# Optimization experiments

Hardware: AMD Instinct MI355X
Metric: run time of the kernel (lower is better)

Reference implementation:

```python
import jax, jax.numpy as jnp
import numpy as np

E4M3_MAX = 448.0
CHUNKS = 4  # module init: chunks=4, seg_mode='weight', equal chunksizes of out//chunks


def fp8_quant(v):
    # Simulate real e4m3 quantization: saturate then round-to-nearest e4m3, back to f32.
    return jnp.clip(v, -E4M3_MAX, E4M3_MAX).astype(jnp.float8_e4m3fn).astype(jnp.float32)


def setup_inputs() -> dict:
    key = jax.random.key(0)
    k1, k2, k3 = jax.random.split(key, 3)
    B, S, IN, OUT = 4, 4096, 4096, 4096
    x = jax.random.normal(k1, (B, S, IN), jnp.float32)
    w = jax.random.normal(k2, (OUT, IN), jnp.float32) * 0.02
    bias = jax.random.normal(k3, (OUT,), jnp.float32) * 0.01
    # Max-calibrated per-tensor scales (quantizer.scale from calibration)
    in_scale = jnp.max(jnp.abs(x)) / E4M3_MAX          # scalar
    wc = w.reshape(CHUNKS, OUT // CHUNKS, IN)
    w_scales = jnp.max(jnp.abs(wc), axis=(1, 2)) / E4M3_MAX  # [CHUNKS]
    return {"x": x, "w": w, "bias": bias, "in_scale": in_scale, "w_scales": w_scales}


def reference(x, w, bias, in_scale, w_scales):
    # seg_mode='weight': split weight along out_features into CHUNKS equal chunks,
    # run scaled e4m3 GEMM per chunk, concat outputs along out dim, add bias.
    OUT, IN = w.shape
    wc = w.reshape(CHUNKS, OUT // CHUNKS, IN)                 # [c, oc, i]
    xq = fp8_quant(x / in_scale)                              # [b, s, i]
    wq = fp8_quant(wc / w_scales[:, None, None])              # [c, oc, i]
    # out_i = (xq @ wq_i^T) * in_scale * w_scale_i  (dequant fused into GEMM epilogue)
    out = jnp.einsum('bsi,coi->bsco', xq, wq)
    out = out * (in_scale * w_scales)[None, None, :, None]
    out = out.reshape(x.shape[0], x.shape[1], OUT)            # concat chunk outputs
    return out + bias
```

## Files before the change

kernel.cpp:

```cpp
#include <hip/hip_runtime.h>
#include <stdint.h>

#define E4M3_MAX 448.0f

typedef float f32x4 __attribute__((ext_vector_type(4)));
typedef int   i32x4 __attribute__((ext_vector_type(4)));
typedef int   i32x8 __attribute__((ext_vector_type(8)));

__device__ __forceinline__ void gload_lds16(const void* g, void* l) {
    __builtin_amdgcn_global_load_lds(
        (__attribute__((address_space(1))) void*)(void*)g,
        (__attribute__((address_space(3))) void*)l,
        16, 0, 0);
}

__device__ __forceinline__ uint32_t quant4(float a, float b, float c, float d) {
    a = fminf(fmaxf(a, -E4M3_MAX), E4M3_MAX);
    b = fminf(fmaxf(b, -E4M3_MAX), E4M3_MAX);
    c = fminf(fmaxf(c, -E4M3_MAX), E4M3_MAX);
    d = fminf(fmaxf(d, -E4M3_MAX), E4M3_MAX);
    int q = 0;
    q = __builtin_amdgcn_cvt_pk_fp8_f32(a, b, q, false);
    q = __builtin_amdgcn_cvt_pk_fp8_f32(c, d, q, true);
    return (uint32_t)q;
}

__global__ void quant_x_kernel(const float* __restrict__ x,
                               const float* __restrict__ scale_p,
                               uint4* __restrict__ xq, int n16) {
    const float inv = 1.0f / scale_p[0];
    const int stride = gridDim.x * blockDim.x;
    for (int i = blockIdx.x * blockDim.x + threadIdx.x; i < n16; i += stride) {
        const float4* p = (const float4*)x + (size_t)i * 4;
        float4 v0 = p[0], v1 = p[1], v2 = p[2], v3 = p[3];
        uint4 q;
        q.x = quant4(v0.x * inv, v0.y * inv, v0.z * inv, v0.w * inv);
        q.y = quant4(v1.x * inv, v1.y * inv, v1.z * inv, v1.w * inv);
        q.z = quant4(v2.x * inv, v2.y * inv, v2.z * inv, v2.w * inv);
        q.w = quant4(v3.x * inv, v3.y * inv, v3.z * inv, v3.w * inv);
        xq[i] = q;
    }
}

__global__ void quant_w_kernel(const float* __restrict__ w,
                               const float* __restrict__ wsc,
                               uint4* __restrict__ wq, int n16, int chunk16) {
    const int stride = gridDim.x * blockDim.x;
    for (int i = blockIdx.x * blockDim.x + threadIdx.x; i < n16; i += stride) {
        const float inv = 1.0f / wsc[i / chunk16];
        const float4* p = (const float4*)w + (size_t)i * 4;
        float4 v0 = p[0], v1 = p[1], v2 = p[2], v3 = p[3];
        uint4 q;
        q.x = quant4(v0.x * inv, v0.y * inv, v0.z * inv, v0.w * inv);
        q.y = quant4(v1.x * inv, v1.y * inv, v1.z * inv, v1.w * inv);
        q.z = quant4(v2.x * inv, v2.y * inv, v2.z * inv, v2.w * inv);
        q.w = quant4(v3.x * inv, v3.y * inv, v3.z * inv, v3.w * inv);
        wq[i] = q;
    }
}

__device__ __forceinline__ i32x8 read_frag(const uint8_t* base, int o0, int o1) {
    i32x4 lo = *(const i32x4*)(base + o0);
    i32x4 hi = *(const i32x4*)(base + o1);
    return __builtin_shufflevector(lo, hi, 0, 1, 2, 3, 4, 5, 6, 7);
}

#define MFMA_MX(a, b, c) \
    __builtin_amdgcn_mfma_scale_f32_16x16x128_f8f6f4( \
        (a), (b), (c), 0, 0, 0, 0x7F7F7F7F, 0, 0x7F7F7F7F)

#define BM 256
#define BN 256
#define BKB 128

__global__ __launch_bounds__(512, 2) void gemm_fp8_kernel(
    const uint8_t* __restrict__ Aq, const uint8_t* __restrict__ Bq,
    const float* __restrict__ bias, const float* __restrict__ isp,
    const float* __restrict__ wsc, float* __restrict__ out,
    int M, int N, int K, int ocPerChunk) {
    __shared__ __align__(16) uint8_t lds[2][2][BM * BKB];

    const int tid  = threadIdx.x;
    const int lane = tid & 63;
    const int wid  = tid >> 6;
    const int wm   = wid >> 2;
    const int wn   = wid & 3;

    const int nwg = gridDim.x;
    const int cpx = nwg >> 3;
    const int swz = (blockIdx.x & 7) * cpx + (blockIdx.x >> 3);
    const int nbx = N / BN;
    const int bx  = swz % nbx;
    const int by  = swz / nbx;
    const int m0  = by * BM;
    const int n0  = bx * BN;

    const int lr   = lane & 15;
    const int sw   = (lr & 7) << 4;
    const int off0 = ((lane >> 4) * 32) ^ sw;
    const int off1 = off0 ^ 16;

    f32x4 acc[8][4] = {};

    const int nkt = K / BKB;

    auto stage = [&](int b, int kt) {
#pragma unroll
        for (int i = 0; i < 8; ++i) {
            const int idx = i * 512 + tid;
            const int row = idx >> 3;
            const int col = ((idx & 7) * 16) ^ ((row & 7) << 4);
            const uint8_t* src = (i < 4)
                ? Aq + (size_t)(m0 + row) * K + kt + col
                : Bq + (size_t)(n0 + (row - 256)) * K + kt + col;
            gload_lds16(src, &lds[b][0][0] + idx * 16);
        }
    };

    stage(0, 0);
    asm volatile("s_waitcnt vmcnt(0)" ::: "memory");
    __builtin_amdgcn_s_barrier();

    for (int t = 0; t < nkt; ++t) {
        const int cur = t & 1;
        const uint8_t* pa = &lds[cur][0][0] + (wm * 128 + lr) * BKB;
        const uint8_t* pb = &lds[cur][1][0] + (wn * 64  + lr) * BKB;

        i32x8 bv[4];
#pragma unroll
        for (int ni = 0; ni < 4; ni++)
            bv[ni] = read_frag(pb + ni * 16 * BKB, off0, off1);
        i32x8 a0 = read_frag(pa,            off0, off1);
        i32x8 a1 = read_frag(pa + 16 * BKB, off0, off1);
        if (t + 1 < nkt) stage(cur ^ 1, (t + 1) * BKB);

        __builtin_amdgcn_s_barrier();
        asm volatile("s_waitcnt lgkmcnt(0)" ::: "memory");
        __builtin_amdgcn_sched_barrier(0);
        __builtin_amdgcn_s_setprio(1);
#pragma unroll
        for (int ni = 0; ni < 4; ni++) {
            acc[0][ni] = MFMA_MX(a0, bv[ni], acc[0][ni]);
            acc[1][ni] = MFMA_MX(a1, bv[ni], acc[1][ni]);
        }
        __builtin_amdgcn_s_setprio(0);

#pragma unroll
        for (int p = 1; p < 4; ++p) {
            i32x8 c0 = read_frag(pa + (2 * p)     * 16 * BKB, off0, off1);
            i32x8 c1 = read_frag(pa + (2 * p + 1) * 16 * BKB, off0, off1);
            __builtin_amdgcn_s_barrier();
            asm volatile("s_waitcnt lgkmcnt(0)" ::: "memory");
            __builtin_amdgcn_sched_barrier(0);
            __builtin_amdgcn_s_setprio(1);
#pragma unroll
            for (int ni = 0; ni < 4; ni++) {
                acc[2 * p][ni]     = MFMA_MX(c0, bv[ni], acc[2 * p][ni]);
                acc[2 * p + 1][ni] = MFMA_MX(c1, bv[ni], acc[2 * p + 1][ni]);
            }
            __builtin_amdgcn_s_setprio(0);
        }

        asm volatile("s_waitcnt vmcnt(0)" ::: "memory");
        __builtin_amdgcn_s_barrier();
    }

    const float is = isp[0];
#pragma unroll
    for (int ni = 0; ni < 4; ni++) {
        const int cidx = n0 + wn * 64 + ni * 16 + lr;
        const float sc = is * wsc[cidx / ocPerChunk];
        const float bs = bias[cidx];
#pragma unroll
        for (int mi = 0; mi < 8; mi++) {
            const int rbase = m0 + wm * 128 + mi * 16 + (lane >> 4) * 4;
#pragma unroll
            for (int j = 0; j < 4; j++)
                out[(size_t)(rbase + j) * N + cidx] = acc[mi][ni][j] * sc + bs;
        }
    }
}

extern "C" void kernel_launch(void* const* d_in, const int* in_sizes, int n_in,
                              void* d_out, int out_size, void* d_ws, size_t ws_size,
                              hipStream_t stream) {
    const float* x        = (const float*)d_in[0];
    const float* w        = (const float*)d_in[1];
    const float* bias     = (const float*)d_in[2];
    const float* in_scale = (const float*)d_in[3];
    const float* w_scales = (const float*)d_in[4];
    float* out = (float*)d_out;

    const int N = in_sizes[2];
    const int K = in_sizes[1] / N;
    const int M = in_sizes[0] / K;
    const int CHUNKS = in_sizes[4];
    const int ocPerChunk = N / CHUNKS;

    uint8_t* xq = (uint8_t*)d_ws;
    uint8_t* wq = xq + (size_t)M * K;

    const int xn16 = (int)(((size_t)M * K) / 16);
    const int wn16 = (int)(((size_t)N * K) / 16);
    const int chunk16 = (N / CHUNKS) * K / 16;

    quant_x_kernel<<<2048, 256, 0, stream>>>(x, in_scale, (uint4*)xq, xn16);
    quant_w_kernel<<<2048, 256, 0, stream>>>(w, w_scales, (uint4*)wq, wn16, chunk16);

    const int nblk = (M / BM) * (N / BN);
    gemm_fp8_kernel<<<dim3(nblk), 512, 0, stream>>>(xq, wq, bias, in_scale,
                                                    w_scales, out, M, N, K,
                                                    ocPerChunk);
}
```

Before: 405.1 us.

## Software-pipeline A-fragment LDS reads with partial lgkmcnt waits in GEMM loop

Reworks the inner K-step so that A fragments for the next MFMA group are read from LDS while the current group runs. Each group now waits only for the older reads (lgkmcnt(4)) instead of draining all LDS traffic. The three intra-iteration workgroup barriers between MFMA phases are removed, leaving the end-of-iteration barrier. This is meant to hide LDS read latency behind matrix math and to cut barrier stalls, at the cost of more live fragment registers. That register pressure could hurt occupancy under the 512x2 launch bounds.

```diff
diff --git a/kernel.cpp b/kernel.cpp
--- a/kernel.cpp
+++ b/kernel.cpp
@@ -69,6 +69,12 @@
     __builtin_amdgcn_mfma_scale_f32_16x16x128_f8f6f4( \
         (a), (b), (c), 0, 0, 0, 0x7F7F7F7F, 0, 0x7F7F7F7F)
 
+#define WAIT_LGKM(n)                                          \
+    do {                                                      \
+        asm volatile("s_waitcnt lgkmcnt(" #n ")" ::: "memory"); \
+        __builtin_amdgcn_sched_barrier(0);                    \
+    } while (0)
+
 #define BM 256
 #define BN 256
 #define BKB 128
@@ -132,11 +138,11 @@
             bv[ni] = read_frag(pb + ni * 16 * BKB, off0, off1);
         i32x8 a0 = read_frag(pa,            off0, off1);
         i32x8 a1 = read_frag(pa + 16 * BKB, off0, off1);
+        i32x8 a2 = read_frag(pa + 32 * BKB, off0, off1);
+        i32x8 a3 = read_frag(pa + 48 * BKB, off0, off1);
         if (t + 1 < nkt) stage(cur ^ 1, (t + 1) * BKB);
 
-        __builtin_amdgcn_s_barrier();
-        asm volatile("s_waitcnt lgkmcnt(0)" ::: "memory");
-        __builtin_amdgcn_sched_barrier(0);
+        WAIT_LGKM(4);
         __builtin_amdgcn_s_setprio(1);
 #pragma unroll
         for (int ni = 0; ni < 4; ni++) {
@@ -145,21 +151,36 @@
         }
         __builtin_amdgcn_s_setprio(0);
 
-#pragma unroll
-        for (int p = 1; p < 4; ++p) {
-            i32x8 c0 = read_frag(pa + (2 * p)     * 16 * BKB, off0, off1);
-            i32x8 c1 = read_frag(pa + (2 * p + 1) * 16 * BKB, off0, off1);
-            __builtin_amdgcn_s_barrier();
-            asm volatile("s_waitcnt lgkmcnt(0)" ::: "memory");
-            __builtin_amdgcn_sched_barrier(0);
-            __builtin_amdgcn_s_setprio(1);
-#pragma unroll
-            for (int ni = 0; ni < 4; ni++) {
-                acc[2 * p][ni]     = MFMA_MX(c0, bv[ni], acc[2 * p][ni]);
-                acc[2 * p + 1][ni] = MFMA_MX(c1, bv[ni], acc[2 * p + 1][ni]);
-            }
-            __builtin_amdgcn_s_setprio(0);
-        }
+        i32x8 a4 = read_frag(pa + 64 * BKB, off0, off1);
+        i32x8 a5 = read_frag(pa + 80 * BKB, off0, off1);
+        WAIT_LGKM(4);
+        __builtin_amdgcn_s_setprio(1);
+#pragma unroll
+        for (int ni = 0; ni < 4; ni++) {
+            acc[2][ni] = MFMA_MX(a2, bv[ni], acc[2][ni]);
+            acc[3][ni] = MFMA_MX(a3, bv[ni], acc[3][ni]);
+        }
+        __builtin_amdgcn_s_setprio(0);
+
+        i32x8 a6 = read_frag(pa + 96 * BKB,  off0, off1);
+        i32x8 a7 = read_frag(pa + 112 * BKB, off0, off1);
+        WAIT_LGKM(4);
+        __builtin_amdgcn_s_setprio(1);
+#pragma unroll
+        for (int ni = 0; ni < 4; ni++) {
+            acc[4][ni] = MFMA_MX(a4, bv[ni], acc[4][ni]);
+            acc[5][ni] = MFMA_MX(a5, bv[ni], acc[5][ni]);
+        }
+        __builtin_amdgcn_s_setprio(0);
+
+        WAIT_LGKM(0);
+        __builtin_amdgcn_s_setprio(1);
+#pragma unroll
+        for (int ni = 0; ni < 4; ni++) {
+            acc[6][ni] = MFMA_MX(a6, bv[ni], acc[6][ni]);
+            acc[7][ni] = MFMA_MX(a7, bv[ni], acc[7][ni]);
+        }
+        __builtin_amdgcn_s_setprio(0);
 
         asm volatile("s_waitcnt vmcnt(0)" ::: "memory");
         __builtin_amdgcn_s_barrier();
```

Result: faster. 372.8 us (median of 3 runs) (-8.0%).
